# Performance work log

Measured on AMD Instinct MI355X. Metric: run time of the kernel, lower is better.

## Reference

```python
import jax, jax.numpy as jnp
import numpy as np

# Model config (mirrors init_kwargs)
E = 8          # num_experts
K = 2          # top_k
S = 1          # select_top_k
THRESHOLD = 0.7
NORM_TOPK = True
H = 1024       # hidden_dim
F = 1024       # moe intermediate dim
B, SEQ = 2, 1024


def setup_inputs() -> dict:
    key = jax.random.key(0)
    k1, k2, k3, k4, k5 = jax.random.split(key, 5)
    hidden_states = jax.random.normal(k1, (B, SEQ, H), jnp.float32)
    gate_weight = jax.random.normal(k2, (E, H), jnp.float32) * 0.02
    gate_up_proj = jax.random.normal(k3, (E, 2 * F, H), jnp.float32) * 0.02
    down_proj = jax.random.normal(k4, (E, H, F), jnp.float32) * 0.02
    sim = jax.random.uniform(k5, (E, E), jnp.float32)
    sim = (sim + sim.T) / 2.0
    sim = sim.at[jnp.arange(E), jnp.arange(E)].set(1.0)  # fill_diagonal_(1.0)
    return {
        "hidden_states": hidden_states,
        "gate_weight": gate_weight,
        "gate_up_proj": gate_up_proj,
        "down_proj": down_proj,
        "similarity_matrix": sim,
    }


def reference(hidden_states, gate_weight, gate_up_proj, down_proj, similarity_matrix):
    b, s, h = hidden_states.shape
    x = hidden_states.reshape(-1, h)                     # [N, H]
    N = x.shape[0]

    # Router: logits -> softmax(fp32) -> topk (+ optional norm)
    logits = x @ gate_weight.T                           # [N, E]
    probs = jax.nn.softmax(logits.astype(jnp.float32), axis=-1)
    top_w, top_i = jax.lax.top_k(probs, K)               # [N, K]
    if NORM_TOPK:
        top_w = top_w / jnp.clip(jnp.sum(top_w, -1, keepdims=True), 1e-12)

    # SERE reroute: primary = union of top-S experts over batch; map each
    # secondary expert to its most-similar primary if sim >= threshold.
    primary_mask = jnp.zeros((E,), bool).at[top_i[:, :S].reshape(-1)].set(True)
    sim = jnp.where(primary_mask[None, :], similarity_matrix.astype(jnp.float32), -jnp.inf)
    best_j = jnp.argmax(sim, axis=-1)                    # best primary per expert
    best_sim = jnp.max(sim, axis=-1)
    ids = jnp.arange(E)
    expert_map = jnp.where((~primary_mask) & (best_sim >= THRESHOLD), best_j, ids)
    rerouted = expert_map[top_i]                         # [N, K]

    # Merge duplicate slots via scatter-add, then re-topk K.
    rows = jnp.arange(N)[:, None]
    dense = jnp.zeros((N, E), top_w.dtype).at[rows, rerouted].add(top_w)
    fw, fi = jax.lax.top_k(dense, K)                     # nnz per row <= K, so topk keeps all
    combine = jnp.zeros((N, E), fw.dtype).at[rows, fi].add(jnp.where(fw > 0, fw, 0.0))  # [N, E]

    # Expert MLPs (dense jit-friendly dispatch): silu(gate)*up -> down
    gu = jnp.einsum('nh,efh->enf', x, gate_up_proj)      # [E, N, 2F]
    g, u = jnp.split(gu, 2, axis=-1)
    hmid = jax.nn.silu(g) * u                            # [E, N, F]
    y = jnp.einsum('enf,ehf->enh', hmid, down_proj)      # [E, N, H]
    out = jnp.einsum('ne,enh->nh', combine, y)           # weighted combine
    return out.reshape(b, s, h)
```

## Files before the change

kernel.cpp:

```cpp
#include <hip/hip_runtime.h>
#include <cstdint>
#include <cstddef>

#define N_TOK 2048
#define HID 1024
#define FDIM 1024
#define NE 8
#define PAIR_CAP 5120
#define MT 128
#define BK 64
#define THRESH 0.7f

typedef __attribute__((ext_vector_type(8))) short bf16x8;
typedef __attribute__((ext_vector_type(4))) float f32x4;

static __device__ __forceinline__ unsigned short f2bf(float f) {
  unsigned int u = __float_as_uint(f);
  u += 0x7FFF + ((u >> 16) & 1);
  return (unsigned short)(u >> 16);
}
static __device__ __forceinline__ float bf2f(unsigned short u) {
  return __uint_as_float(((unsigned int)u) << 16);
}

static __device__ __forceinline__ void gl2lds16(const unsigned short* g, unsigned short* l) {
  __builtin_amdgcn_global_load_lds(
      (const __attribute__((address_space(1))) void*)g,
      (__attribute__((address_space(3))) void*)l, 16, 0, 0);
}

__global__ __launch_bounds__(256) void k_cvt2(
    const float* __restrict__ a, unsigned short* __restrict__ ab, int n4a,
    const float* __restrict__ b, unsigned short* __restrict__ bb, int n4b) {
  int i = blockIdx.x * 256 + threadIdx.x;
  if (i < n4a) {
    float4 v = ((const float4*)a)[i];
    ushort4 o;
    o.x = f2bf(v.x); o.y = f2bf(v.y); o.z = f2bf(v.z); o.w = f2bf(v.w);
    ((ushort4*)ab)[i] = o;
  } else {
    int j = i - n4a;
    if (j < n4b) {
      float4 v = ((const float4*)b)[j];
      ushort4 o;
      o.x = f2bf(v.x); o.y = f2bf(v.y); o.z = f2bf(v.z); o.w = f2bf(v.w);
      ((ushort4*)bb)[j] = o;
    }
  }
}

__global__ __launch_bounds__(256) void k_router(
    const float* __restrict__ x, const float* __restrict__ gw,
    unsigned short* __restrict__ xb, float* __restrict__ topw,
    int* __restrict__ topi) {
  __shared__ float sgw[NE * HID];
  int t = threadIdx.x;
#pragma unroll
  for (int i = 0; i < NE * HID / 256; ++i) sgw[t + 256 * i] = gw[t + 256 * i];
  __syncthreads();
  int lane = t & 63;
  int wave = t >> 6;
  int n = blockIdx.x * 4 + wave;
  float acc[NE];
#pragma unroll
  for (int e = 0; e < NE; ++e) acc[e] = 0.f;
#pragma unroll
  for (int i = 0; i < HID / 64; ++i) {
    int h = i * 64 + lane;
    float xv = x[(size_t)n * HID + h];
    xb[(size_t)n * HID + h] = f2bf(xv);
#pragma unroll
    for (int e = 0; e < NE; ++e) acc[e] += xv * sgw[e * HID + h];
  }
#pragma unroll
  for (int off = 32; off > 0; off >>= 1) {
#pragma unroll
    for (int e = 0; e < NE; ++e) acc[e] += __shfl_xor(acc[e], off, 64);
  }
  if (lane == 0) {
    float m = acc[0];
    for (int e = 1; e < NE; ++e) m = fmaxf(m, acc[e]);
    float p[NE]; float s = 0.f;
    for (int e = 0; e < NE; ++e) { p[e] = __expf(acc[e] - m); s += p[e]; }
    float inv = 1.f / s;
    for (int e = 0; e < NE; ++e) p[e] *= inv;
    int i0 = 0; float b0 = p[0];
    for (int e = 1; e < NE; ++e) if (p[e] > b0) { b0 = p[e]; i0 = e; }
    int i1 = -1; float b1 = -1.f;
    for (int e = 0; e < NE; ++e) { if (e == i0) continue; if (p[e] > b1) { b1 = p[e]; i1 = e; } }
    float sw = b0 + b1; if (sw < 1e-12f) sw = 1e-12f;
    topw[n * 2] = b0 / sw; topw[n * 2 + 1] = b1 / sw;
    topi[n * 2] = i0;      topi[n * 2 + 1] = i1;
  }
}

__global__ __launch_bounds__(256) void k_pairs(
    const float* __restrict__ sim, const int* __restrict__ topi,
    const float* __restrict__ topw, int* __restrict__ ctrl,
    int* __restrict__ ptok, float* __restrict__ pw, int* __restrict__ pot) {
  __shared__ int prim[NE], emap[NE], cnt[NE], soff[NE], cur[NE], padc[NE];
  int t = threadIdx.x;
  if (t < NE) { prim[t] = 0; cnt[t] = 0; }
  __syncthreads();
  for (int n = t; n < N_TOK; n += 256) prim[topi[n * 2]] = 1;
  __syncthreads();
  if (t < NE) {
    float best = -1e30f; int bj = -1;
    for (int j = 0; j < NE; ++j) {
      if (prim[j]) {
        float s = sim[t * NE + j];
        if (s > best) { best = s; bj = j; }
      }
    }
    int m = t;
    if (!prim[t] && bj >= 0 && best >= THRESH) m = bj;
    emap[t] = m;
  }
  __syncthreads();
  for (int n = t; n < N_TOK; n += 256) {
    atomicAdd(&cnt[emap[topi[n * 2]]], 1);
    atomicAdd(&cnt[emap[topi[n * 2 + 1]]], 1);
  }
  __syncthreads();
  if (t == 0) {
    int o = 0;
    for (int e = 0; e < NE; ++e) {
      soff[e] = o;
      int p = (cnt[e] + MT - 1) & ~(MT - 1);
      padc[e] = p; cur[e] = 0; o += p;
    }
  }
  __syncthreads();
  if (t < NE) { ctrl[24 + t] = soff[t]; ctrl[32 + t] = padc[t]; }
  for (int n = t; n < N_TOK; n += 256) {
    int i0 = topi[n * 2], i1 = topi[n * 2 + 1];
    int e0 = emap[i0], e1 = emap[i1];
    int s0 = soff[e0] + atomicAdd(&cur[e0], 1);
    int s1 = soff[e1] + atomicAdd(&cur[e1], 1);
    ptok[s0] = n; pw[s0] = topw[n * 2];
    ptok[s1] = n; pw[s1] = topw[n * 2 + 1];
    pot[n * 2] = s0; pot[n * 2 + 1] = s1;
  }
  __syncthreads();
  for (int e = 0; e < NE; ++e) {
    for (int s = cnt[e] + t; s < padc[e]; s += 256) {
      ptok[soff[e] + s] = 0; pw[soff[e] + s] = 0.f;
    }
  }
}


__global__ __launch_bounds__(256, 2) void k_gemm1(
    const unsigned short* __restrict__ xb, const unsigned short* __restrict__ gupb,
    unsigned short* __restrict__ hmid, const int* __restrict__ ptok,
    const int* __restrict__ ctrl) {
  int b = blockIdx.x;
  int mt = b >> 7;
  int r7 = b & 127;
  int e = r7 >> 4;
  int y = r7 & 15;
  int padc = ctrl[32 + e];
  if (mt * MT >= padc) return;
  int base = ctrl[24 + e] + mt * MT;
  int f0 = y * 64;

  __shared__ unsigned short As[MT * BK];
  __shared__ unsigned short Bs[128 * BK];
  __shared__ int toks[MT];

  int t = threadIdx.x;
  if (t < MT) toks[t] = ptok[base + t];
  __syncthreads();

  int lane = t & 63;
  int wave = t >> 6;
  int wm = wave >> 1, wn = wave & 1;
  int lm = lane & 15, lh = lane >> 4;

  f32x4 acc[4][4] = {};
  const unsigned short* gbase = gupb + (size_t)e * 2 * FDIM * HID;

  for (int k0 = 0; k0 < HID; k0 += BK) {
#pragma unroll
    for (int i = 0; i < 4; ++i) {
      int q = i * 256 + t;
      int r = q >> 3;
      int cl = (q & 7) ^ (r & 7);
      gl2lds16(xb + (size_t)toks[r] * HID + k0 + cl * 8, &As[(q & ~63) * 8]);
    }
#pragma unroll
    for (int i = 0; i < 4; ++i) {
      int q = i * 256 + t;
      int r = q >> 3;
      int cl = (q & 7) ^ (r & 7);
      int grow = ((r >> 4) & 1) * FDIM + f0 + ((r >> 5) << 4) + (r & 15);
      gl2lds16(gbase + (size_t)grow * HID + k0 + cl * 8, &Bs[(q & ~63) * 8]);
    }
    __syncthreads();
#pragma unroll
    for (int kk = 0; kk < 2; ++kk) {
      bf16x8 af[4], bfr[4];
#pragma unroll
      for (int rb = 0; rb < 4; ++rb) {
        int row = wm * 64 + rb * 16 + lm;
        int p = (kk * 4 + lh) ^ (row & 7);
        af[rb] = *(const bf16x8*)(&As[row * BK + p * 8]);
      }
#pragma unroll
      for (int cc = 0; cc < 4; ++cc) {
        int row = wn * 64 + cc * 16 + lm;
        int p = (kk * 4 + lh) ^ (row & 7);
        bfr[cc] = *(const bf16x8*)(&Bs[row * BK + p * 8]);
      }
#pragma unroll
      for (int rb = 0; rb < 4; ++rb) {
#pragma unroll
        for (int cc = 0; cc < 4; ++cc)
          acc[rb][cc] = __builtin_amdgcn_mfma_f32_16x16x32_bf16(af[rb], bfr[cc], acc[rb][cc], 0, 0, 0);
      }
    }
    __syncthreads();
  }
#pragma unroll
  for (int rb = 0; rb < 4; ++rb) {
    int slot = base + wm * 64 + rb * 16 + lh * 4;
#pragma unroll
    for (int fb = 0; fb < 2; ++fb) {
      f32x4 g = acc[rb][fb * 2];
      f32x4 u = acc[rb][fb * 2 + 1];
      int f = f0 + wn * 32 + fb * 16 + lm;
#pragma unroll
      for (int reg = 0; reg < 4; ++reg) {
        float gv = g[reg];
        float hm = gv / (1.f + __expf(-gv)) * u[reg];
        hmid[(size_t)(slot + reg) * FDIM + f] = f2bf(hm);
      }
    }
  }
}

__global__ __launch_bounds__(256, 2) void k_gemm2(
    const unsigned short* __restrict__ hmid, const unsigned short* __restrict__ dwnb,
    unsigned short* __restrict__ yb, const int* __restrict__ ctrl) {
  int b = blockIdx.x;
  int mt = b >> 6;
  int r6 = b & 63;
  int e = r6 >> 3;
  int y = r6 & 7;
  int padc = ctrl[32 + e];
  if (mt * MT >= padc) return;
  int base = ctrl[24 + e] + mt * MT;
  int h0 = y * 128;

  __shared__ unsigned short As[MT * BK];
  __shared__ unsigned short Bs[128 * BK];

  int t = threadIdx.x;
  int lane = t & 63;
  int wave = t >> 6;
  int wm = wave >> 1, wn = wave & 1;
  int lm = lane & 15, lh = lane >> 4;

  f32x4 acc[4][4] = {};
  const unsigned short* dbase = dwnb + (size_t)e * HID * FDIM;

  for (int k0 = 0; k0 < FDIM; k0 += BK) {
#pragma unroll
    for (int i = 0; i < 4; ++i) {
      int q = i * 256 + t;
      int r = q >> 3;
      int cl = (q & 7) ^ (r & 7);
      gl2lds16(hmid + (size_t)(base + r) * FDIM + k0 + cl * 8, &As[(q & ~63) * 8]);
    }
#pragma unroll
    for (int i = 0; i < 4; ++i) {
      int q = i * 256 + t;
      int r = q >> 3;
      int cl = (q & 7) ^ (r & 7);
      gl2lds16(dbase + (size_t)(h0 + r) * FDIM + k0 + cl * 8, &Bs[(q & ~63) * 8]);
    }
    __syncthreads();
#pragma unroll
    for (int kk = 0; kk < 2; ++kk) {
      bf16x8 af[4], bfr[4];
#pragma unroll
      for (int rb = 0; rb < 4; ++rb) {
        int row = wm * 64 + rb * 16 + lm;
        int p = (kk * 4 + lh) ^ (row & 7);
        af[rb] = *(const bf16x8*)(&As[row * BK + p * 8]);
      }
#pragma unroll
      for (int cc = 0; cc < 4; ++cc) {
        int row = wn * 64 + cc * 16 + lm;
        int p = (kk * 4 + lh) ^ (row & 7);
        bfr[cc] = *(const bf16x8*)(&Bs[row * BK + p * 8]);
      }
#pragma unroll
      for (int rb = 0; rb < 4; ++rb) {
#pragma unroll
        for (int cc = 0; cc < 4; ++cc)
          acc[rb][cc] = __builtin_amdgcn_mfma_f32_16x16x32_bf16(af[rb], bfr[cc], acc[rb][cc], 0, 0, 0);
      }
    }
    __syncthreads();
  }
#pragma unroll
  for (int rb = 0; rb < 4; ++rb) {
    int slot = base + wm * 64 + rb * 16 + lh * 4;
#pragma unroll
    for (int cc = 0; cc < 4; ++cc) {
      int h = h0 + wn * 64 + cc * 16 + lm;
#pragma unroll
      for (int reg = 0; reg < 4; ++reg)
        yb[(size_t)(slot + reg) * HID + h] = f2bf(acc[rb][cc][reg]);
    }
  }
}

__global__ __launch_bounds__(256) void k_combine(
    const unsigned short* __restrict__ yb, const float* __restrict__ pw,
    const int* __restrict__ pot, float* __restrict__ out) {
  int n = blockIdx.x;
  int t = threadIdx.x;
  int p0 = pot[n * 2], p1 = pot[n * 2 + 1];
  float w0 = pw[p0], w1 = pw[p1];
  int h = t * 4;
  ushort4 a = *(const ushort4*)(yb + (size_t)p0 * HID + h);
  ushort4 b = *(const ushort4*)(yb + (size_t)p1 * HID + h);
  float4 o;
  o.x = w0 * bf2f(a.x) + w1 * bf2f(b.x);
  o.y = w0 * bf2f(a.y) + w1 * bf2f(b.y);
  o.z = w0 * bf2f(a.z) + w1 * bf2f(b.z);
  o.w = w0 * bf2f(a.w) + w1 * bf2f(b.w);
  *(float4*)(out + (size_t)n * HID + h) = o;
}

extern "C" void kernel_launch(void* const* d_in, const int* in_sizes, int n_in,
                              void* d_out, int out_size, void* d_ws, size_t ws_size,
                              hipStream_t stream) {
  (void)in_sizes; (void)n_in; (void)out_size; (void)ws_size;
  const float* x   = (const float*)d_in[0];
  const float* gw  = (const float*)d_in[1];
  const float* gup = (const float*)d_in[2];
  const float* dwn = (const float*)d_in[3];
  const float* sim = (const float*)d_in[4];
  float* out = (float*)d_out;

  char* w = (char*)d_ws;
  int* ctrl = (int*)w;
  size_t off = 256;
  unsigned short* xb = (unsigned short*)(w + off); off += (size_t)N_TOK * HID * 2;
  float* topw = (float*)(w + off); off += (size_t)N_TOK * 2 * 4;
  int*   topi = (int*)(w + off);   off += (size_t)N_TOK * 2 * 4;
  int*   ptok = (int*)(w + off);   off += (size_t)PAIR_CAP * 4;
  float* pw   = (float*)(w + off); off += (size_t)PAIR_CAP * 4;
  int*   pot  = (int*)(w + off);   off += (size_t)N_TOK * 2 * 4;
  unsigned short* hmid = (unsigned short*)(w + off); off += (size_t)PAIR_CAP * FDIM * 2;
  unsigned short* yb   = (unsigned short*)(w + off); off += (size_t)PAIR_CAP * HID * 2;
  unsigned short* gupb = (unsigned short*)(w + off); off += (size_t)NE * 2 * FDIM * HID * 2;
  unsigned short* dwnb = (unsigned short*)(w + off); off += (size_t)NE * HID * FDIM * 2;

  int n4g = NE * 2 * FDIM * HID / 4;
  int n4d = NE * HID * FDIM / 4;
  k_cvt2<<<(n4g + n4d + 255) / 256, 256, 0, stream>>>(gup, gupb, n4g, dwn, dwnb, n4d);
  k_router<<<N_TOK / 4, 256, 0, stream>>>(x, gw, xb, topw, topi);
  k_pairs<<<1, 256, 0, stream>>>(sim, topi, topw, ctrl, ptok, pw, pot);
  k_gemm1<<<dim3(32 * 128), 256, 0, stream>>>(xb, gupb, hmid, ptok, ctrl);
  k_gemm2<<<dim3(32 * 64), 256, 0, stream>>>(hmid, dwnb, yb, ctrl);
  k_combine<<<N_TOK, 256, 0, stream>>>(yb, pw, pot, out);
}
```

Before: 201.9 us.

## Compact tile worklist, split-K gemm2 with atomic scatter into output, drop combine kernel

The pairing kernel now emits a compact list of (expert, m-tile) work items, so the GEMM kernels launch only as many blocks as there are real tiles instead of a worst-case grid that exits early. The down-projection GEMM splits K in two and writes weighted results straight into the fp32 output with atomicAdd, after a memset. This removes the bf16 intermediate y buffer and the separate combine kernel. In exchange it adds a memset and atomic traffic to the output, and the order of floating-point sums is no longer deterministic.

```diff
diff --git a/kernel.cpp b/kernel.cpp
--- a/kernel.cpp
+++ b/kernel.cpp
@@ -124,11 +124,14 @@
   __syncthreads();
   if (t == 0) {
     int o = 0;
+    int w = 0;
     for (int e = 0; e < NE; ++e) {
       soff[e] = o;
       int p = (cnt[e] + MT - 1) & ~(MT - 1);
       padc[e] = p; cur[e] = 0; o += p;
-    }
+      for (int m = 0; m < p / MT; ++m) ctrl[40 + w++] = (e << 16) | m;
+    }
+    ctrl[1] = w;
   }
   __syncthreads();
   if (t < NE) { ctrl[24 + t] = soff[t]; ctrl[32 + t] = padc[t]; }
@@ -155,12 +158,12 @@
     unsigned short* __restrict__ hmid, const int* __restrict__ ptok,
     const int* __restrict__ ctrl) {
   int b = blockIdx.x;
-  int mt = b >> 7;
-  int r7 = b & 127;
-  int e = r7 >> 4;
-  int y = r7 & 15;
-  int padc = ctrl[32 + e];
-  if (mt * MT >= padc) return;
+  int i4 = b >> 4;
+  if (i4 >= ctrl[1]) return;
+  int wlv = ctrl[40 + i4];
+  int e = wlv >> 16;
+  int mt = wlv & 0xffff;
+  int y = b & 15;
   int base = ctrl[24 + e] + mt * MT;
   int f0 = y * 64;
 
@@ -241,21 +244,28 @@
 
 __global__ __launch_bounds__(256, 2) void k_gemm2(
     const unsigned short* __restrict__ hmid, const unsigned short* __restrict__ dwnb,
-    unsigned short* __restrict__ yb, const int* __restrict__ ctrl) {
+    const int* __restrict__ ptok, const float* __restrict__ pw,
+    float* __restrict__ out, const int* __restrict__ ctrl) {
   int b = blockIdx.x;
-  int mt = b >> 6;
-  int r6 = b & 63;
-  int e = r6 >> 3;
-  int y = r6 & 7;
-  int padc = ctrl[32 + e];
-  if (mt * MT >= padc) return;
+  int i4 = b >> 4;
+  if (i4 >= ctrl[1]) return;
+  int wlv = ctrl[40 + i4];
+  int e = wlv >> 16;
+  int mt = wlv & 0xffff;
+  int sub = b & 15;
+  int ks = sub >> 3;
+  int y = sub & 7;
   int base = ctrl[24 + e] + mt * MT;
   int h0 = y * 128;
 
   __shared__ unsigned short As[MT * BK];
   __shared__ unsigned short Bs[128 * BK];
+  __shared__ int toks[MT];
+  __shared__ float pws[MT];
 
   int t = threadIdx.x;
+  if (t < MT) { toks[t] = ptok[base + t]; pws[t] = pw[base + t]; }
+
   int lane = t & 63;
   int wave = t >> 6;
   int wm = wave >> 1, wn = wave & 1;
@@ -264,7 +274,8 @@
   f32x4 acc[4][4] = {};
   const unsigned short* dbase = dwnb + (size_t)e * HID * FDIM;
 
-  for (int k0 = 0; k0 < FDIM; k0 += BK) {
+  int kbeg = ks * (FDIM / 2);
+  for (int k0 = kbeg; k0 < kbeg + FDIM / 2; k0 += BK) {
 #pragma unroll
     for (int i = 0; i < 4; ++i) {
       int q = i * 256 + t;
@@ -306,39 +317,27 @@
   }
 #pragma unroll
   for (int rb = 0; rb < 4; ++rb) {
-    int slot = base + wm * 64 + rb * 16 + lh * 4;
-#pragma unroll
-    for (int cc = 0; cc < 4; ++cc) {
-      int h = h0 + wn * 64 + cc * 16 + lm;
-#pragma unroll
-      for (int reg = 0; reg < 4; ++reg)
-        yb[(size_t)(slot + reg) * HID + h] = f2bf(acc[rb][cc][reg]);
-    }
-  }
-}
-
-__global__ __launch_bounds__(256) void k_combine(
-    const unsigned short* __restrict__ yb, const float* __restrict__ pw,
-    const int* __restrict__ pot, float* __restrict__ out) {
-  int n = blockIdx.x;
-  int t = threadIdx.x;
-  int p0 = pot[n * 2], p1 = pot[n * 2 + 1];
-  float w0 = pw[p0], w1 = pw[p1];
-  int h = t * 4;
-  ushort4 a = *(const ushort4*)(yb + (size_t)p0 * HID + h);
-  ushort4 b = *(const ushort4*)(yb + (size_t)p1 * HID + h);
-  float4 o;
-  o.x = w0 * bf2f(a.x) + w1 * bf2f(b.x);
-  o.y = w0 * bf2f(a.y) + w1 * bf2f(b.y);
-  o.z = w0 * bf2f(a.z) + w1 * bf2f(b.z);
-  o.w = w0 * bf2f(a.w) + w1 * bf2f(b.w);
-  *(float4*)(out + (size_t)n * HID + h) = o;
+    int sl0 = wm * 64 + rb * 16 + lh * 4;
+#pragma unroll
+    for (int reg = 0; reg < 4; ++reg) {
+      int sl = sl0 + reg;
+      float wgt = pws[sl];
+      if (wgt != 0.f) {
+        float* orow = out + (size_t)toks[sl] * HID;
+#pragma unroll
+        for (int cc = 0; cc < 4; ++cc) {
+          int h = h0 + wn * 64 + cc * 16 + lm;
+          atomicAdd(orow + h, wgt * acc[rb][cc][reg]);
+        }
+      }
+    }
+  }
 }
 
 extern "C" void kernel_launch(void* const* d_in, const int* in_sizes, int n_in,
                               void* d_out, int out_size, void* d_ws, size_t ws_size,
                               hipStream_t stream) {
-  (void)in_sizes; (void)n_in; (void)out_size; (void)ws_size;
+  (void)in_sizes; (void)n_in; (void)ws_size;
   const float* x   = (const float*)d_in[0];
   const float* gw  = (const float*)d_in[1];
   const float* gup = (const float*)d_in[2];
@@ -348,7 +347,7 @@
 
   char* w = (char*)d_ws;
   int* ctrl = (int*)w;
-  size_t off = 256;
+  size_t off = 512;
   unsigned short* xb = (unsigned short*)(w + off); off += (size_t)N_TOK * HID * 2;
   float* topw = (float*)(w + off); off += (size_t)N_TOK * 2 * 4;
   int*   topi = (int*)(w + off);   off += (size_t)N_TOK * 2 * 4;
@@ -356,7 +355,6 @@
   float* pw   = (float*)(w + off); off += (size_t)PAIR_CAP * 4;
   int*   pot  = (int*)(w + off);   off += (size_t)N_TOK * 2 * 4;
   unsigned short* hmid = (unsigned short*)(w + off); off += (size_t)PAIR_CAP * FDIM * 2;
-  unsigned short* yb   = (unsigned short*)(w + off); off += (size_t)PAIR_CAP * HID * 2;
   unsigned short* gupb = (unsigned short*)(w + off); off += (size_t)NE * 2 * FDIM * HID * 2;
   unsigned short* dwnb = (unsigned short*)(w + off); off += (size_t)NE * HID * FDIM * 2;
 
@@ -365,7 +363,7 @@
   k_cvt2<<<(n4g + n4d + 255) / 256, 256, 0, stream>>>(gup, gupb, n4g, dwn, dwnb, n4d);
   k_router<<<N_TOK / 4, 256, 0, stream>>>(x, gw, xb, topw, topi);
   k_pairs<<<1, 256, 0, stream>>>(sim, topi, topw, ctrl, ptok, pw, pot);
-  k_gemm1<<<dim3(32 * 128), 256, 0, stream>>>(xb, gupb, hmid, ptok, ctrl);
-  k_gemm2<<<dim3(32 * 64), 256, 0, stream>>>(hmid, dwnb, yb, ctrl);
-  k_combine<<<N_TOK, 256, 0, stream>>>(yb, pw, pot, out);
-}
+  hipMemsetAsync(out, 0, (size_t)N_TOK * HID * sizeof(float), stream);
+  k_gemm1<<<dim3(40 * 16), 256, 0, stream>>>(xb, gupb, hmid, ptok, ctrl);
+  k_gemm2<<<dim3(40 * 16), 256, 0, stream>>>(hmid, dwnb, ptok, pw, out, ctrl);
+}
```

New measurement: 219.8 us. 8.9% more time.

## Fuse all MoE stages into one persistent kernel with grid barriers

Applied to the files above, without the earlier changes.

Replaces the six separate launches (convert, router, pair build, two GEMMs, combine) with a single persistent kernel of 512 blocks that moves between phases through atomic grid-wide barriers. The down-projection weight conversion is overlapped with the single-block pair construction, and the GEMM phases iterate over a compact work list of only the populated expert tiles. This removes launch gaps and empty-block launches, but relies on all 512 blocks being co-resident, adds barrier spin costs, and has a spin cap that could break correctness if blocks are not co-resident.

```diff
diff --git a/kernel.cpp b/kernel.cpp
--- a/kernel.cpp
+++ b/kernel.cpp
@@ -10,6 +10,7 @@
 #define MT 128
 #define BK 64
 #define THRESH 0.7f
+#define NBLK 512
 
 typedef __attribute__((ext_vector_type(8))) short bf16x8;
 typedef __attribute__((ext_vector_type(4))) float f32x4;
@@ -29,310 +30,316 @@
       (__attribute__((address_space(3))) void*)l, 16, 0, 0);
 }
 
-__global__ __launch_bounds__(256) void k_cvt2(
-    const float* __restrict__ a, unsigned short* __restrict__ ab, int n4a,
-    const float* __restrict__ b, unsigned short* __restrict__ bb, int n4b) {
-  int i = blockIdx.x * 256 + threadIdx.x;
-  if (i < n4a) {
-    float4 v = ((const float4*)a)[i];
-    ushort4 o;
-    o.x = f2bf(v.x); o.y = f2bf(v.y); o.z = f2bf(v.z); o.w = f2bf(v.w);
-    ((ushort4*)ab)[i] = o;
-  } else {
-    int j = i - n4a;
-    if (j < n4b) {
-      float4 v = ((const float4*)b)[j];
+static __device__ __forceinline__ void gridbar(int* bar, int idx) {
+  __syncthreads();
+  if (threadIdx.x == 0) {
+    __threadfence();
+    atomicAdd(&bar[idx], 1);
+    int spins = 0;
+    while (__hip_atomic_load(&bar[idx], __ATOMIC_RELAXED,
+                             __HIP_MEMORY_SCOPE_AGENT) < NBLK) {
+      __builtin_amdgcn_s_sleep(8);
+      if (++spins > (1 << 21)) break;
+    }
+    __threadfence();
+  }
+  __syncthreads();
+}
+
+__global__ __launch_bounds__(256, 2) void k_fused(
+    const float* __restrict__ x, const float* __restrict__ gw,
+    const float* __restrict__ gup, const float* __restrict__ dwn,
+    const float* __restrict__ sim, float* __restrict__ out,
+    int* __restrict__ ctrl, unsigned short* __restrict__ xb,
+    float* __restrict__ topw, int* __restrict__ topi,
+    int* __restrict__ ptok, float* __restrict__ pw, int* __restrict__ pot,
+    unsigned short* __restrict__ hmid, unsigned short* __restrict__ yb,
+    unsigned short* __restrict__ gupb, unsigned short* __restrict__ dwnb) {
+  __shared__ __align__(16) unsigned char smem[MT * BK * 2 + 128 * BK * 2 + 512];
+  unsigned short* As = (unsigned short*)smem;
+  unsigned short* Bs = As + MT * BK;
+  int* toks = (int*)(smem + MT * BK * 2 + 128 * BK * 2);
+  int* bar = ctrl + 8;
+
+  int t = threadIdx.x;
+  int bid = blockIdx.x;
+  int lane = t & 63;
+  int wave = t >> 6;
+  int lm = lane & 15, lh = lane >> 4;
+  int wm = wave >> 1, wn = wave & 1;
+
+  {
+    float* sgw = (float*)smem;
+#pragma unroll
+    for (int i = 0; i < NE * HID / 256; ++i) sgw[t + 256 * i] = gw[t + 256 * i];
+    __syncthreads();
+    int n = bid * 4 + wave;
+    float acc[NE];
+#pragma unroll
+    for (int e = 0; e < NE; ++e) acc[e] = 0.f;
+#pragma unroll
+    for (int i = 0; i < HID / 64; ++i) {
+      int h = i * 64 + lane;
+      float xv = x[(size_t)n * HID + h];
+      xb[(size_t)n * HID + h] = f2bf(xv);
+#pragma unroll
+      for (int e = 0; e < NE; ++e) acc[e] += xv * sgw[e * HID + h];
+    }
+#pragma unroll
+    for (int off = 32; off > 0; off >>= 1) {
+#pragma unroll
+      for (int e = 0; e < NE; ++e) acc[e] += __shfl_xor(acc[e], off, 64);
+    }
+    if (lane == 0) {
+      float m = acc[0];
+      for (int e = 1; e < NE; ++e) m = fmaxf(m, acc[e]);
+      float p[NE]; float s = 0.f;
+      for (int e = 0; e < NE; ++e) { p[e] = __expf(acc[e] - m); s += p[e]; }
+      float inv = 1.f / s;
+      for (int e = 0; e < NE; ++e) p[e] *= inv;
+      int i0 = 0; float b0 = p[0];
+      for (int e = 1; e < NE; ++e) if (p[e] > b0) { b0 = p[e]; i0 = e; }
+      int i1 = -1; float b1 = -1.f;
+      for (int e = 0; e < NE; ++e) { if (e == i0) continue; if (p[e] > b1) { b1 = p[e]; i1 = e; } }
+      float sw = b0 + b1; if (sw < 1e-12f) sw = 1e-12f;
+      topw[n * 2] = b0 / sw; topw[n * 2 + 1] = b1 / sw;
+      topi[n * 2] = i0;      topi[n * 2 + 1] = i1;
+    }
+  }
+  {
+    const int n4g = NE * 2 * FDIM * HID / 4;
+    for (int i = bid * 256 + t; i < n4g; i += NBLK * 256) {
+      float4 v = ((const float4*)gup)[i];
       ushort4 o;
       o.x = f2bf(v.x); o.y = f2bf(v.y); o.z = f2bf(v.z); o.w = f2bf(v.w);
-      ((ushort4*)bb)[j] = o;
-    }
-  }
-}
-
-__global__ __launch_bounds__(256) void k_router(
-    const float* __restrict__ x, const float* __restrict__ gw,
-    unsigned short* __restrict__ xb, float* __restrict__ topw,
-    int* __restrict__ topi) {
-  __shared__ float sgw[NE * HID];
-  int t = threadIdx.x;
-#pragma unroll
-  for (int i = 0; i < NE * HID / 256; ++i) sgw[t + 256 * i] = gw[t + 256 * i];
-  __syncthreads();
-  int lane = t & 63;
-  int wave = t >> 6;
-  int n = blockIdx.x * 4 + wave;
-  float acc[NE];
-#pragma unroll
-  for (int e = 0; e < NE; ++e) acc[e] = 0.f;
-#pragma unroll
-  for (int i = 0; i < HID / 64; ++i) {
-    int h = i * 64 + lane;
-    float xv = x[(size_t)n * HID + h];
-    xb[(size_t)n * HID + h] = f2bf(xv);
-#pragma unroll
-    for (int e = 0; e < NE; ++e) acc[e] += xv * sgw[e * HID + h];
-  }
-#pragma unroll
-  for (int off = 32; off > 0; off >>= 1) {
-#pragma unroll
-    for (int e = 0; e < NE; ++e) acc[e] += __shfl_xor(acc[e], off, 64);
-  }
-  if (lane == 0) {
-    float m = acc[0];
-    for (int e = 1; e < NE; ++e) m = fmaxf(m, acc[e]);
-    float p[NE]; float s = 0.f;
-    for (int e = 0; e < NE; ++e) { p[e] = __expf(acc[e] - m); s += p[e]; }
-    float inv = 1.f / s;
-    for (int e = 0; e < NE; ++e) p[e] *= inv;
-    int i0 = 0; float b0 = p[0];
-    for (int e = 1; e < NE; ++e) if (p[e] > b0) { b0 = p[e]; i0 = e; }
-    int i1 = -1; float b1 = -1.f;
-    for (int e = 0; e < NE; ++e) { if (e == i0) continue; if (p[e] > b1) { b1 = p[e]; i1 = e; } }
-    float sw = b0 + b1; if (sw < 1e-12f) sw = 1e-12f;
-    topw[n * 2] = b0 / sw; topw[n * 2 + 1] = b1 / sw;
-    topi[n * 2] = i0;      topi[n * 2 + 1] = i1;
-  }
-}
-
-__global__ __launch_bounds__(256) void k_pairs(
-    const float* __restrict__ sim, const int* __restrict__ topi,
-    const float* __restrict__ topw, int* __restrict__ ctrl,
-    int* __restrict__ ptok, float* __restrict__ pw, int* __restrict__ pot) {
-  __shared__ int prim[NE], emap[NE], cnt[NE], soff[NE], cur[NE], padc[NE];
-  int t = threadIdx.x;
-  if (t < NE) { prim[t] = 0; cnt[t] = 0; }
-  __syncthreads();
-  for (int n = t; n < N_TOK; n += 256) prim[topi[n * 2]] = 1;
-  __syncthreads();
-  if (t < NE) {
-    float best = -1e30f; int bj = -1;
-    for (int j = 0; j < NE; ++j) {
-      if (prim[j]) {
-        float s = sim[t * NE + j];
-        if (s > best) { best = s; bj = j; }
-      }
-    }
-    int m = t;
-    if (!prim[t] && bj >= 0 && best >= THRESH) m = bj;
-    emap[t] = m;
-  }
-  __syncthreads();
-  for (int n = t; n < N_TOK; n += 256) {
-    atomicAdd(&cnt[emap[topi[n * 2]]], 1);
-    atomicAdd(&cnt[emap[topi[n * 2 + 1]]], 1);
-  }
-  __syncthreads();
-  if (t == 0) {
-    int o = 0;
+      ((ushort4*)gupb)[i] = o;
+    }
+  }
+  gridbar(bar, 0);
+
+  if (bid == 0) {
+    __shared__ int prim[NE], emap[NE], cnt[NE], soff[NE], cur[NE], padc[NE];
+    if (t < NE) { prim[t] = 0; cnt[t] = 0; }
+    __syncthreads();
+    for (int n = t; n < N_TOK; n += 256) prim[topi[n * 2]] = 1;
+    __syncthreads();
+    if (t < NE) {
+      float best = -1e30f; int bj = -1;
+      for (int j = 0; j < NE; ++j) {
+        if (prim[j]) {
+          float s = sim[t * NE + j];
+          if (s > best) { best = s; bj = j; }
+        }
+      }
+      int m = t;
+      if (!prim[t] && bj >= 0 && best >= THRESH) m = bj;
+      emap[t] = m;
+    }
+    __syncthreads();
+    for (int n = t; n < N_TOK; n += 256) {
+      atomicAdd(&cnt[emap[topi[n * 2]]], 1);
+      atomicAdd(&cnt[emap[topi[n * 2 + 1]]], 1);
+    }
+    __syncthreads();
+    if (t == 0) {
+      int o = 0;
+      int w = 0;
+      for (int e = 0; e < NE; ++e) {
+        soff[e] = o;
+        int p = (cnt[e] + MT - 1) & ~(MT - 1);
+        padc[e] = p; cur[e] = 0; o += p;
+        for (int m = 0; m < p / MT; ++m) ctrl[40 + w++] = (e << 16) | m;
+      }
+      ctrl[1] = w;
+    }
+    __syncthreads();
+    if (t < NE) { ctrl[24 + t] = soff[t]; ctrl[32 + t] = padc[t]; }
+    for (int n = t; n < N_TOK; n += 256) {
+      int i0 = topi[n * 2], i1 = topi[n * 2 + 1];
+      int e0 = emap[i0], e1 = emap[i1];
+      int s0 = soff[e0] + atomicAdd(&cur[e0], 1);
+      int s1 = soff[e1] + atomicAdd(&cur[e1], 1);
+      ptok[s0] = n; pw[s0] = topw[n * 2];
+      ptok[s1] = n; pw[s1] = topw[n * 2 + 1];
+      pot[n * 2] = s0; pot[n * 2 + 1] = s1;
+    }
+    __syncthreads();
     for (int e = 0; e < NE; ++e) {
-      soff[e] = o;
-      int p = (cnt[e] + MT - 1) & ~(MT - 1);
-      padc[e] = p; cur[e] = 0; o += p;
-    }
-  }
-  __syncthreads();
-  if (t < NE) { ctrl[24 + t] = soff[t]; ctrl[32 + t] = padc[t]; }
-  for (int n = t; n < N_TOK; n += 256) {
-    int i0 = topi[n * 2], i1 = topi[n * 2 + 1];
-    int e0 = emap[i0], e1 = emap[i1];
-    int s0 = soff[e0] + atomicAdd(&cur[e0], 1);
-    int s1 = soff[e1] + atomicAdd(&cur[e1], 1);
-    ptok[s0] = n; pw[s0] = topw[n * 2];
-    ptok[s1] = n; pw[s1] = topw[n * 2 + 1];
-    pot[n * 2] = s0; pot[n * 2 + 1] = s1;
-  }
-  __syncthreads();
-  for (int e = 0; e < NE; ++e) {
-    for (int s = cnt[e] + t; s < padc[e]; s += 256) {
-      ptok[soff[e] + s] = 0; pw[soff[e] + s] = 0.f;
-    }
-  }
-}
-
-
-__global__ __launch_bounds__(256, 2) void k_gemm1(
-    const unsigned short* __restrict__ xb, const unsigned short* __restrict__ gupb,
-    unsigned short* __restrict__ hmid, const int* __restrict__ ptok,
-    const int* __restrict__ ctrl) {
-  int b = blockIdx.x;
-  int mt = b >> 7;
-  int r7 = b & 127;
-  int e = r7 >> 4;
-  int y = r7 & 15;
-  int padc = ctrl[32 + e];
-  if (mt * MT >= padc) return;
-  int base = ctrl[24 + e] + mt * MT;
-  int f0 = y * 64;
-
-  __shared__ unsigned short As[MT * BK];
-  __shared__ unsigned short Bs[128 * BK];
-  __shared__ int toks[MT];
-
-  int t = threadIdx.x;
-  if (t < MT) toks[t] = ptok[base + t];
-  __syncthreads();
-
-  int lane = t & 63;
-  int wave = t >> 6;
-  int wm = wave >> 1, wn = wave & 1;
-  int lm = lane & 15, lh = lane >> 4;
-
-  f32x4 acc[4][4] = {};
-  const unsigned short* gbase = gupb + (size_t)e * 2 * FDIM * HID;
-
-  for (int k0 = 0; k0 < HID; k0 += BK) {
-#pragma unroll
-    for (int i = 0; i < 4; ++i) {
-      int q = i * 256 + t;
-      int r = q >> 3;
-      int cl = (q & 7) ^ (r & 7);
-      gl2lds16(xb + (size_t)toks[r] * HID + k0 + cl * 8, &As[(q & ~63) * 8]);
-    }
-#pragma unroll
-    for (int i = 0; i < 4; ++i) {
-      int q = i * 256 + t;
-      int r = q >> 3;
-      int cl = (q & 7) ^ (r & 7);
-      int grow = ((r >> 4) & 1) * FDIM + f0 + ((r >> 5) << 4) + (r & 15);
-      gl2lds16(gbase + (size_t)grow * HID + k0 + cl * 8, &Bs[(q & ~63) * 8]);
-    }
-    __syncthreads();
-#pragma unroll
-    for (int kk = 0; kk < 2; ++kk) {
-      bf16x8 af[4], bfr[4];
-#pragma unroll
-      for (int rb = 0; rb < 4; ++rb) {
-        int row = wm * 64 + rb * 16 + lm;
-        int p = (kk * 4 + lh) ^ (row & 7);
-        af[rb] = *(const bf16x8*)(&As[row * BK + p * 8]);
-      }
+      for (int s = cnt[e] + t; s < padc[e]; s += 256) {
+        ptok[soff[e] + s] = 0; pw[soff[e] + s] = 0.f;
+      }
+    }
+  } else {
+    const int n4d = NE * HID * FDIM / 4;
+    for (int i = (bid - 1) * 256 + t; i < n4d; i += (NBLK - 1) * 256) {
+      float4 v = ((const float4*)dwn)[i];
+      ushort4 o;
+      o.x = f2bf(v.x); o.y = f2bf(v.y); o.z = f2bf(v.z); o.w = f2bf(v.w);
+      ((ushort4*)dwnb)[i] = o;
+    }
+  }
+  gridbar(bar, 1);
+
+  int nmt = ctrl[1];
+
+  for (int wi = bid; wi < nmt * 16; wi += NBLK) {
+    int i4 = wi >> 4;
+    int wlv = ctrl[40 + i4];
+    int e = wlv >> 16;
+    int mt = wlv & 0xffff;
+    int y = wi & 15;
+    int base = ctrl[24 + e] + mt * MT;
+    int f0 = y * 64;
+
+    if (t < MT) toks[t] = ptok[base + t];
+    __syncthreads();
+
+    f32x4 acc[4][4] = {};
+    const unsigned short* gbase = gupb + (size_t)e * 2 * FDIM * HID;
+
+    for (int k0 = 0; k0 < HID; k0 += BK) {
+#pragma unroll
+      for (int i = 0; i < 4; ++i) {
+        int q = i * 256 + t;
+        int r = q >> 3;
+        int cl = (q & 7) ^ (r & 7);
+        gl2lds16(xb + (size_t)toks[r] * HID + k0 + cl * 8, &As[(q & ~63) * 8]);
+      }
+#pragma unroll
+      for (int i = 0; i < 4; ++i) {
+        int q = i * 256 + t;
+        int r = q >> 3;
+        int cl = (q & 7) ^ (r & 7);
+        int grow = ((r >> 4) & 1) * FDIM + f0 + ((r >> 5) << 4) + (r & 15);
+        gl2lds16(gbase + (size_t)grow * HID + k0 + cl * 8, &Bs[(q & ~63) * 8]);
+      }
+      __syncthreads();
+#pragma unroll
+      for (int kk = 0; kk < 2; ++kk) {
+        bf16x8 af[4], bfr[4];
+#pragma unroll
+        for (int rb = 0; rb < 4; ++rb) {
+          int row = wm * 64 + rb * 16 + lm;
+          int p = (kk * 4 + lh) ^ (row & 7);
+          af[rb] = *(const bf16x8*)(&As[row * BK + p * 8]);
+        }
+#pragma unroll
+        for (int cc = 0; cc < 4; ++cc) {
+          int row = wn * 64 + cc * 16 + lm;
+          int p = (kk * 4 + lh) ^ (row & 7);
+          bfr[cc] = *(const bf16x8*)(&Bs[row * BK + p * 8]);
+        }
+#pragma unroll
+        for (int rb = 0; rb < 4; ++rb) {
+#pragma unroll
+          for (int cc = 0; cc < 4; ++cc)
+            acc[rb][cc] = __builtin_amdgcn_mfma_f32_16x16x32_bf16(af[rb], bfr[cc], acc[rb][cc], 0, 0, 0);
+        }
+      }
+      __syncthreads();
+    }
+#pragma unroll
+    for (int rb = 0; rb < 4; ++rb) {
+      int slot = base + wm * 64 + rb * 16 + lh * 4;
+#pragma unroll
+      for (int fb = 0; fb < 2; ++fb) {
+        f32x4 g = acc[rb][fb * 2];
+        f32x4 u = acc[rb][fb * 2 + 1];
+        int f = f0 + wn * 32 + fb * 16 + lm;
+#pragma unroll
+        for (int reg = 0; reg < 4; ++reg) {
+          float gv = g[reg];
+          float hm = gv / (1.f + __expf(-gv)) * u[reg];
+          hmid[(size_t)(slot + reg) * FDIM + f] = f2bf(hm);
+        }
+      }
+    }
+    __syncthreads();
+  }
+  gridbar(bar, 2);
+
+  for (int wi = bid; wi < nmt * 8; wi += NBLK) {
+    int i4 = wi >> 3;
+    int wlv = ctrl[40 + i4];
+    int e = wlv >> 16;
+    int mt = wlv & 0xffff;
+    int y = wi & 7;
+    int base = ctrl[24 + e] + mt * MT;
+    int h0 = y * 128;
+
+    f32x4 acc[4][4] = {};
+    const unsigned short* dbase = dwnb + (size_t)e * HID * FDIM;
+
+    for (int k0 = 0; k0 < FDIM; k0 += BK) {
+#pragma unroll
+      for (int i = 0; i < 4; ++i) {
+        int q = i * 256 + t;
+        int r = q >> 3;
+        int cl = (q & 7) ^ (r & 7);
+        gl2lds16(hmid + (size_t)(base + r) * FDIM + k0 + cl * 8, &As[(q & ~63) * 8]);
+      }
+#pragma unroll
+      for (int i = 0; i < 4; ++i) {
+        int q = i * 256 + t;
+        int r = q >> 3;
+        int cl = (q & 7) ^ (r & 7);
+        gl2lds16(dbase + (size_t)(h0 + r) * FDIM + k0 + cl * 8, &Bs[(q & ~63) * 8]);
+      }
+      __syncthreads();
+#pragma unroll
+      for (int kk = 0; kk < 2; ++kk) {
+        bf16x8 af[4], bfr[4];
+#pragma unroll
+        for (int rb = 0; rb < 4; ++rb) {
+          int row = wm * 64 + rb * 16 + lm;
+          int p = (kk * 4 + lh) ^ (row & 7);
+          af[rb] = *(const bf16x8*)(&As[row * BK + p * 8]);
+        }
+#pragma unroll
+        for (int cc = 0; cc < 4; ++cc) {
+          int row = wn * 64 + cc * 16 + lm;
+          int p = (kk * 4 + lh) ^ (row & 7);
+          bfr[cc] = *(const bf16x8*)(&Bs[row * BK + p * 8]);
+        }
+#pragma unroll
+        for (int rb = 0; rb < 4; ++rb) {
+#pragma unroll
+          for (int cc = 0; cc < 4; ++cc)
+            acc[rb][cc] = __builtin_amdgcn_mfma_f32_16x16x32_bf16(af[rb], bfr[cc], acc[rb][cc], 0, 0, 0);
+        }
+      }
+      __syncthreads();
+    }
+#pragma unroll
+    for (int rb = 0; rb < 4; ++rb) {
+      int slot = base + wm * 64 + rb * 16 + lh * 4;
 #pragma unroll
       for (int cc = 0; cc < 4; ++cc) {
-        int row = wn * 64 + cc * 16 + lm;
-        int p = (kk * 4 + lh) ^ (row & 7);
-        bfr[cc] = *(const bf16x8*)(&Bs[row * BK + p * 8]);
-      }
-#pragma unroll
-      for (int rb = 0; rb < 4; ++rb) {
-#pragma unroll
-        for (int cc = 0; cc < 4; ++cc)
-          acc[rb][cc] = __builtin_amdgcn_mfma_f32_16x16x32_bf16(af[rb], bfr[cc], acc[rb][cc], 0, 0, 0);
-      }
-    }
-    __syncthreads();
-  }
-#pragma unroll
-  for (int rb = 0; rb < 4; ++rb) {
-    int slot = base + wm * 64 + rb * 16 + lh * 4;
-#pragma unroll
-    for (int fb = 0; fb < 2; ++fb) {
-      f32x4 g = acc[rb][fb * 2];
-      f32x4 u = acc[rb][fb * 2 + 1];
-      int f = f0 + wn * 32 + fb * 16 + lm;
-#pragma unroll
-      for (int reg = 0; reg < 4; ++reg) {
-        float gv = g[reg];
-        float hm = gv / (1.f + __expf(-gv)) * u[reg];
-        hmid[(size_t)(slot + reg) * FDIM + f] = f2bf(hm);
-      }
-    }
-  }
-}
-
-__global__ __launch_bounds__(256, 2) void k_gemm2(
-    const unsigned short* __restrict__ hmid, const unsigned short* __restrict__ dwnb,
-    unsigned short* __restrict__ yb, const int* __restrict__ ctrl) {
-  int b = blockIdx.x;
-  int mt = b >> 6;
-  int r6 = b & 63;
-  int e = r6 >> 3;
-  int y = r6 & 7;
-  int padc = ctrl[32 + e];
-  if (mt * MT >= padc) return;
-  int base = ctrl[24 + e] + mt * MT;
-  int h0 = y * 128;
-
-  __shared__ unsigned short As[MT * BK];
-  __shared__ unsigned short Bs[128 * BK];
-
-  int t = threadIdx.x;
-  int lane = t & 63;
-  int wave = t >> 6;
-  int wm = wave >> 1, wn = wave & 1;
-  int lm = lane & 15, lh = lane >> 4;
-
-  f32x4 acc[4][4] = {};
-  const unsigned short* dbase = dwnb + (size_t)e * HID * FDIM;
-
-  for (int k0 = 0; k0 < FDIM; k0 += BK) {
-#pragma unroll
-    for (int i = 0; i < 4; ++i) {
-      int q = i * 256 + t;
-      int r = q >> 3;
-      int cl = (q & 7) ^ (r & 7);
-      gl2lds16(hmid + (size_t)(base + r) * FDIM + k0 + cl * 8, &As[(q & ~63) * 8]);
-    }
-#pragma unroll
-    for (int i = 0; i < 4; ++i) {
-      int q = i * 256 + t;
-      int r = q >> 3;
-      int cl = (q & 7) ^ (r & 7);
-      gl2lds16(dbase + (size_t)(h0 + r) * FDIM + k0 + cl * 8, &Bs[(q & ~63) * 8]);
-    }
-    __syncthreads();
-#pragma unroll
-    for (int kk = 0; kk < 2; ++kk) {
-      bf16x8 af[4], bfr[4];
-#pragma unroll
-      for (int rb = 0; rb < 4; ++rb) {
-        int row = wm * 64 + rb * 16 + lm;
-        int p = (kk * 4 + lh) ^ (row & 7);
-        af[rb] = *(const bf16x8*)(&As[row * BK + p * 8]);
-      }
-#pragma unroll
-      for (int cc = 0; cc < 4; ++cc) {
-        int row = wn * 64 + cc * 16 + lm;
-        int p = (kk * 4 + lh) ^ (row & 7);
-        bfr[cc] = *(const bf16x8*)(&Bs[row * BK + p * 8]);
-      }
-#pragma unroll
-      for (int rb = 0; rb < 4; ++rb) {
-#pragma unroll
-        for (int cc = 0; cc < 4; ++cc)
-          acc[rb][cc] = __builtin_amdgcn_mfma_f32_16x16x32_bf16(af[rb], bfr[cc], acc[rb][cc], 0, 0, 0);
-      }
-    }
-    __syncthreads();
-  }
-#pragma unroll
-  for (int rb = 0; rb < 4; ++rb) {
-    int slot = base + wm * 64 + rb * 16 + lh * 4;
-#pragma unroll
-    for (int cc = 0; cc < 4; ++cc) {
-      int h = h0 + wn * 64 + cc * 16 + lm;
-#pragma unroll
-      for (int reg = 0; reg < 4; ++reg)
-        yb[(size_t)(slot + reg) * HID + h] = f2bf(acc[rb][cc][reg]);
-    }
-  }
-}
-
-__global__ __launch_bounds__(256) void k_combine(
-    const unsigned short* __restrict__ yb, const float* __restrict__ pw,
-    const int* __restrict__ pot, float* __restrict__ out) {
-  int n = blockIdx.x;
-  int t = threadIdx.x;
-  int p0 = pot[n * 2], p1 = pot[n * 2 + 1];
-  float w0 = pw[p0], w1 = pw[p1];
-  int h = t * 4;
-  ushort4 a = *(const ushort4*)(yb + (size_t)p0 * HID + h);
-  ushort4 b = *(const ushort4*)(yb + (size_t)p1 * HID + h);
-  float4 o;
-  o.x = w0 * bf2f(a.x) + w1 * bf2f(b.x);
-  o.y = w0 * bf2f(a.y) + w1 * bf2f(b.y);
-  o.z = w0 * bf2f(a.z) + w1 * bf2f(b.z);
-  o.w = w0 * bf2f(a.w) + w1 * bf2f(b.w);
-  *(float4*)(out + (size_t)n * HID + h) = o;
+        int h = h0 + wn * 64 + cc * 16 + lm;
+#pragma unroll
+        for (int reg = 0; reg < 4; ++reg)
+          yb[(size_t)(slot + reg) * HID + h] = f2bf(acc[rb][cc][reg]);
+      }
+    }
+    __syncthreads();
+  }
+  gridbar(bar, 3);
+
+#pragma unroll
+  for (int tk = 0; tk < 4; ++tk) {
+    int n = bid * 4 + tk;
+    int p0 = pot[n * 2], p1 = pot[n * 2 + 1];
+    float w0 = pw[p0], w1 = pw[p1];
+    int h = t * 4;
+    ushort4 a = *(const ushort4*)(yb + (size_t)p0 * HID + h);
+    ushort4 b = *(const ushort4*)(yb + (size_t)p1 * HID + h);
+    float4 o;
+    o.x = w0 * bf2f(a.x) + w1 * bf2f(b.x);
+    o.y = w0 * bf2f(a.y) + w1 * bf2f(b.y);
+    o.z = w0 * bf2f(a.z) + w1 * bf2f(b.z);
+    o.w = w0 * bf2f(a.w) + w1 * bf2f(b.w);
+    *(float4*)(out + (size_t)n * HID + h) = o;
+  }
 }
 
 extern "C" void kernel_launch(void* const* d_in, const int* in_sizes, int n_in,
@@ -348,7 +355,7 @@
 
   char* w = (char*)d_ws;
   int* ctrl = (int*)w;
-  size_t off = 256;
+  size_t off = 512;
   unsigned short* xb = (unsigned short*)(w + off); off += (size_t)N_TOK * HID * 2;
   float* topw = (float*)(w + off); off += (size_t)N_TOK * 2 * 4;
   int*   topi = (int*)(w + off);   off += (size_t)N_TOK * 2 * 4;
@@ -360,12 +367,8 @@
   unsigned short* gupb = (unsigned short*)(w + off); off += (size_t)NE * 2 * FDIM * HID * 2;
   unsigned short* dwnb = (unsigned short*)(w + off); off += (size_t)NE * HID * FDIM * 2;
 
-  int n4g = NE * 2 * FDIM * HID / 4;
-  int n4d = NE * HID * FDIM / 4;
-  k_cvt2<<<(n4g + n4d + 255) / 256, 256, 0, stream>>>(gup, gupb, n4g, dwn, dwnb, n4d);
-  k_router<<<N_TOK / 4, 256, 0, stream>>>(x, gw, xb, topw, topi);
-  k_pairs<<<1, 256, 0, stream>>>(sim, topi, topw, ctrl, ptok, pw, pot);
-  k_gemm1<<<dim3(32 * 128), 256, 0, stream>>>(xb, gupb, hmid, ptok, ctrl);
-  k_gemm2<<<dim3(32 * 64), 256, 0, stream>>>(hmid, dwnb, yb, ctrl);
-  k_combine<<<N_TOK, 256, 0, stream>>>(yb, pw, pot, out);
-}
+  hipMemsetAsync(ctrl, 0, 512, stream);
+  k_fused<<<dim3(NBLK), dim3(256), 0, stream>>>(
+      x, gw, gup, dwn, sim, out, ctrl, xb, topw, topi,
+      ptok, pw, pot, hmid, yb, gupb, dwnb);
+}
```

New measurement: 432.0 us. +114.0%, slower.

## Fuse weight bf16 conversion into GEMM loads and compact grid via work list

Applied to the files above, without the earlier changes.

Drops the separate fp32->bf16 conversion pass over both expert weight tensors and converts the fp32 weights inline while staging B tiles into LDS in both GEMMs. It also builds a compact list of (expert, m-tile) work items in the pairing kernel so the GEMM grids only launch active tiles instead of many early-exiting blocks. This removes a full read/write pass over about 100MB of weights, but each GEMM block now reads fp32 weights with synchronous register loads instead of async global-to-LDS copies, and the same weight tiles are re-read and re-converted by every m-tile.

```diff
diff --git a/kernel.cpp b/kernel.cpp
--- a/kernel.cpp
+++ b/kernel.cpp
@@ -29,24 +29,15 @@
       (__attribute__((address_space(3))) void*)l, 16, 0, 0);
 }
 
-__global__ __launch_bounds__(256) void k_cvt2(
-    const float* __restrict__ a, unsigned short* __restrict__ ab, int n4a,
-    const float* __restrict__ b, unsigned short* __restrict__ bb, int n4b) {
-  int i = blockIdx.x * 256 + threadIdx.x;
-  if (i < n4a) {
-    float4 v = ((const float4*)a)[i];
-    ushort4 o;
-    o.x = f2bf(v.x); o.y = f2bf(v.y); o.z = f2bf(v.z); o.w = f2bf(v.w);
-    ((ushort4*)ab)[i] = o;
-  } else {
-    int j = i - n4a;
-    if (j < n4b) {
-      float4 v = ((const float4*)b)[j];
-      ushort4 o;
-      o.x = f2bf(v.x); o.y = f2bf(v.y); o.z = f2bf(v.z); o.w = f2bf(v.w);
-      ((ushort4*)bb)[j] = o;
-    }
-  }
+static __device__ __forceinline__ bf16x8 ld8cvt(const float* g) {
+  float4 v0 = *(const float4*)g;
+  float4 v1 = *(const float4*)(g + 4);
+  bf16x8 o;
+  o[0] = (short)f2bf(v0.x); o[1] = (short)f2bf(v0.y);
+  o[2] = (short)f2bf(v0.z); o[3] = (short)f2bf(v0.w);
+  o[4] = (short)f2bf(v1.x); o[5] = (short)f2bf(v1.y);
+  o[6] = (short)f2bf(v1.z); o[7] = (short)f2bf(v1.w);
+  return o;
 }
 
 __global__ __launch_bounds__(256) void k_router(
@@ -124,11 +115,14 @@
   __syncthreads();
   if (t == 0) {
     int o = 0;
+    int w = 0;
     for (int e = 0; e < NE; ++e) {
       soff[e] = o;
       int p = (cnt[e] + MT - 1) & ~(MT - 1);
       padc[e] = p; cur[e] = 0; o += p;
-    }
+      for (int m = 0; m < p / MT; ++m) ctrl[40 + w++] = (e << 16) | m;
+    }
+    ctrl[1] = w;
   }
   __syncthreads();
   if (t < NE) { ctrl[24 + t] = soff[t]; ctrl[32 + t] = padc[t]; }
@@ -151,16 +145,16 @@
 
 
 __global__ __launch_bounds__(256, 2) void k_gemm1(
-    const unsigned short* __restrict__ xb, const unsigned short* __restrict__ gupb,
+    const unsigned short* __restrict__ xb, const float* __restrict__ gup,
     unsigned short* __restrict__ hmid, const int* __restrict__ ptok,
     const int* __restrict__ ctrl) {
   int b = blockIdx.x;
-  int mt = b >> 7;
-  int r7 = b & 127;
-  int e = r7 >> 4;
-  int y = r7 & 15;
-  int padc = ctrl[32 + e];
-  if (mt * MT >= padc) return;
+  int i4 = b >> 4;
+  if (i4 >= ctrl[1]) return;
+  int wlv = ctrl[40 + i4];
+  int e = wlv >> 16;
+  int mt = wlv & 0xffff;
+  int y = b & 15;
   int base = ctrl[24 + e] + mt * MT;
   int f0 = y * 64;
 
@@ -178,7 +172,7 @@
   int lm = lane & 15, lh = lane >> 4;
 
   f32x4 acc[4][4] = {};
-  const unsigned short* gbase = gupb + (size_t)e * 2 * FDIM * HID;
+  const float* gbase = gup + (size_t)e * 2 * FDIM * HID;
 
   for (int k0 = 0; k0 < HID; k0 += BK) {
 #pragma unroll
@@ -194,7 +188,8 @@
       int r = q >> 3;
       int cl = (q & 7) ^ (r & 7);
       int grow = ((r >> 4) & 1) * FDIM + f0 + ((r >> 5) << 4) + (r & 15);
-      gl2lds16(gbase + (size_t)grow * HID + k0 + cl * 8, &Bs[(q & ~63) * 8]);
+      bf16x8 o = ld8cvt(gbase + (size_t)grow * HID + k0 + cl * 8);
+      *(bf16x8*)(&Bs[q * 8]) = o;
     }
     __syncthreads();
 #pragma unroll
@@ -240,15 +235,15 @@
 }
 
 __global__ __launch_bounds__(256, 2) void k_gemm2(
-    const unsigned short* __restrict__ hmid, const unsigned short* __restrict__ dwnb,
+    const unsigned short* __restrict__ hmid, const float* __restrict__ dwn,
     unsigned short* __restrict__ yb, const int* __restrict__ ctrl) {
   int b = blockIdx.x;
-  int mt = b >> 6;
-  int r6 = b & 63;
-  int e = r6 >> 3;
-  int y = r6 & 7;
-  int padc = ctrl[32 + e];
-  if (mt * MT >= padc) return;
+  int i4 = b >> 3;
+  if (i4 >= ctrl[1]) return;
+  int wlv = ctrl[40 + i4];
+  int e = wlv >> 16;
+  int mt = wlv & 0xffff;
+  int y = b & 7;
   int base = ctrl[24 + e] + mt * MT;
   int h0 = y * 128;
 
@@ -262,7 +257,7 @@
   int lm = lane & 15, lh = lane >> 4;
 
   f32x4 acc[4][4] = {};
-  const unsigned short* dbase = dwnb + (size_t)e * HID * FDIM;
+  const float* dbase = dwn + (size_t)e * HID * FDIM;
 
   for (int k0 = 0; k0 < FDIM; k0 += BK) {
 #pragma unroll
@@ -277,7 +272,8 @@
       int q = i * 256 + t;
       int r = q >> 3;
       int cl = (q & 7) ^ (r & 7);
-      gl2lds16(dbase + (size_t)(h0 + r) * FDIM + k0 + cl * 8, &Bs[(q & ~63) * 8]);
+      bf16x8 o = ld8cvt(dbase + (size_t)(h0 + r) * FDIM + k0 + cl * 8);
+      *(bf16x8*)(&Bs[q * 8]) = o;
     }
     __syncthreads();
 #pragma unroll
@@ -348,7 +344,7 @@
 
   char* w = (char*)d_ws;
   int* ctrl = (int*)w;
-  size_t off = 256;
+  size_t off = 512;
   unsigned short* xb = (unsigned short*)(w + off); off += (size_t)N_TOK * HID * 2;
   float* topw = (float*)(w + off); off += (size_t)N_TOK * 2 * 4;
   int*   topi = (int*)(w + off);   off += (size_t)N_TOK * 2 * 4;
@@ -357,15 +353,10 @@
   int*   pot  = (int*)(w + off);   off += (size_t)N_TOK * 2 * 4;
   unsigned short* hmid = (unsigned short*)(w + off); off += (size_t)PAIR_CAP * FDIM * 2;
   unsigned short* yb   = (unsigned short*)(w + off); off += (size_t)PAIR_CAP * HID * 2;
-  unsigned short* gupb = (unsigned short*)(w + off); off += (size_t)NE * 2 * FDIM * HID * 2;
-  unsigned short* dwnb = (unsigned short*)(w + off); off += (size_t)NE * HID * FDIM * 2;
-
-  int n4g = NE * 2 * FDIM * HID / 4;
-  int n4d = NE * HID * FDIM / 4;
-  k_cvt2<<<(n4g + n4d + 255) / 256, 256, 0, stream>>>(gup, gupb, n4g, dwn, dwnb, n4d);
+
   k_router<<<N_TOK / 4, 256, 0, stream>>>(x, gw, xb, topw, topi);
   k_pairs<<<1, 256, 0, stream>>>(sim, topi, topw, ctrl, ptok, pw, pot);
-  k_gemm1<<<dim3(32 * 128), 256, 0, stream>>>(xb, gupb, hmid, ptok, ctrl);
-  k_gemm2<<<dim3(32 * 64), 256, 0, stream>>>(hmid, dwnb, yb, ctrl);
+  k_gemm1<<<dim3(40 * 16), 256, 0, stream>>>(xb, gup, hmid, ptok, ctrl);
+  k_gemm2<<<dim3(40 * 8), 256, 0, stream>>>(hmid, dwn, yb, ctrl);
   k_combine<<<N_TOK, 256, 0, stream>>>(yb, pw, pot, out);
 }
```

After: 209.8 us. 1.04x slower.
